# Optimization experiments

Hardware: AMD Instinct MI355X
Metric: run time of the kernel (lower is better)

The kernel has to match this reference:

```python
import jax, jax.numpy as jnp
import numpy as np

N = 1_000_000          # number of RoIs
C = 4                  # num_class (foreground classes)
IMG_H, IMG_W = 1080.0, 1920.0
BBOX_MEAN = jnp.array([0.0, 0.0, 0.0, 0.0], jnp.float32)
BBOX_STD = jnp.array([0.1, 0.1, 0.2, 0.2], jnp.float32)
THR_OBJ = 0.2          # threshold_objectness
THR_CLS = 0.1          # thresholds[0]
MIN_W, MIN_H = 6.0, 6.0
MAX_CAND = 300         # nms max_candidate_n
OVERLAP = 0.5          # nms overlap_ratio
TOP_N = 100            # nms top_n


def setup_inputs() -> dict:
    key = jax.random.key(0)
    k1, k2, k3, k4, k5 = jax.random.split(key, 5)
    logits = jax.random.normal(k1, (N, C + 1), jnp.float32) * 2.0
    cls_score_softmax = jax.nn.softmax(logits, axis=-1)          # rows sum to 1, like softmax output
    bbox_pred = jax.random.normal(k2, (N, 4 * (C + 1)), jnp.float32) * 0.5
    x1 = jax.random.uniform(k3, (N,), jnp.float32, 0.0, IMG_W * 0.8)
    y1 = jax.random.uniform(k4, (N,), jnp.float32, 0.0, IMG_H * 0.8)
    wh = jax.random.uniform(k5, (N, 2), jnp.float32, 8.0, 200.0)
    rois = jnp.stack([jnp.zeros((N,), jnp.float32), x1, y1, x1 + wh[:, 0], y1 + wh[:, 1]], axis=1)
    im_info = jnp.array([IMG_H, IMG_W], jnp.float32)
    return {"cls_score_softmax": cls_score_softmax, "bbox_pred": bbox_pred, "rois": rois, "im_info": im_info}


def _pairwise_iou(b):
    # torchvision box_iou convention: area = (x2-x1)*(y2-y1), no +1
    lt = jnp.maximum(b[:, None, :2], b[None, :, :2])
    rb = jnp.minimum(b[:, None, 2:], b[None, :, 2:])
    wh = jnp.clip(rb - lt, 0.0)
    inter = wh[..., 0] * wh[..., 1]
    area = (b[:, 2] - b[:, 0]) * (b[:, 3] - b[:, 1])
    return inter / (area[:, None] + area[None, :] - inter)


def _forward(cls_score_softmax, bbox_pred, rois, im_info):
    h_img, w_img = im_info[0], im_info[1]
    # denormalize deltas and decode against rois (bbox_transform_inv_rcnn)
    deltas = (bbox_pred.reshape(-1, 4) * BBOX_STD + BBOX_MEAN).reshape(-1, C + 1, 4)
    bx = rois[:, 1:]
    w = bx[:, 2] - bx[:, 0] + 1.0
    h = bx[:, 3] - bx[:, 1] + 1.0
    cx = bx[:, 0] + 0.5 * (w - 1.0)
    cy = bx[:, 1] + 0.5 * (h - 1.0)
    pcx = deltas[:, :, 0] * w[:, None] + cx[:, None]
    pcy = deltas[:, :, 1] * h[:, None] + cy[:, None]
    pw = jnp.exp(deltas[:, :, 2]) * w[:, None]
    ph = jnp.exp(deltas[:, :, 3]) * h[:, None]
    pred = jnp.stack([pcx - 0.5 * (pw - 1.0), pcy - 0.5 * (ph - 1.0),
                      pcx + 0.5 * (pw - 1.0), pcy + 0.5 * (ph - 1.0)], axis=-1)  # [N, C+1, 4]
    # refine_out_of_map_bbox: clip to image
    pred = jnp.stack([jnp.clip(pred[..., 0], 0.0, w_img - 1.0),
                      jnp.clip(pred[..., 1], 0.0, h_img - 1.0),
                      jnp.clip(pred[..., 2], 0.0, w_img - 1.0),
                      jnp.clip(pred[..., 3], 0.0, h_img - 1.0)], axis=-1)
    # objectness + class-score filters (masked instead of compacted: jit-friendly)
    mask_obj = (1.0 - cls_score_softmax[:, 0]) >= THR_OBJ
    maxes = jnp.max(cls_score_softmax[:, 1:], axis=1)
    argmaxes = jnp.argmax(cls_score_softmax[:, 1:], axis=1) + 1
    mask_cls = maxes > THR_CLS
    # select the box of the argmax class per row
    box = jnp.take_along_axis(pred, argmaxes[:, None, None], axis=1)[:, 0, :]  # [N, 4]
    bw = box[:, 2] - box[:, 0] + 1.0
    bh = box[:, 3] - box[:, 1] + 1.0
    mask_size = (bw >= MIN_W) | (bh >= MIN_H)  # HEIGHT_OR_WIDTH
    valid = mask_obj & mask_cls & mask_size
    # top-k candidates by max class prob (invalid rows pushed below any real score)
    cand_scores = jnp.where(valid, maxes, -1.0)
    top_vals, top_idx = jax.lax.top_k(cand_scores, MAX_CAND)   # sorted descending
    cand_boxes = box[top_idx]                                   # [M, 4]
    cand_probs = cls_score_softmax[top_idx]                     # [M, C+1]
    cand_valid = top_vals > -0.5
    # greedy NMS over the (score-sorted) candidates
    iou = _pairwise_iou(cand_boxes)
    idx = jnp.arange(MAX_CAND)

    def body(i, keep):
        sup = keep[i] & (iou[i] > OVERLAP) & (idx > i)
        return keep & ~sup

    keep = jax.lax.fori_loop(0, MAX_CAND, body, cand_valid)
    # compact kept rows into the first TOP_N slots (drop-row scatter trick)
    order = jnp.cumsum(keep.astype(jnp.int32)) - 1
    slot = jnp.where(keep & (order < TOP_N), order, TOP_N)
    rows = jnp.concatenate([jnp.zeros((MAX_CAND, 1), cand_boxes.dtype), cand_boxes, cand_probs], axis=1)
    out = jnp.zeros((TOP_N + 1, rows.shape[1]), rows.dtype).at[slot].set(rows)[:TOP_N]
    return out  # [TOP_N, 1 + 4 + (C+1)] = [100, 10], zero-padded past the kept count


def reference(cls_score_softmax, bbox_pred, rois, im_info):
    return _forward(cls_score_softmax, bbox_pred, rois, im_info)
```

## Files before the change

### kernel.cpp

```cpp
#include <hip/hip_runtime.h>
#include <math.h>

#define NBINS 4096
#define CAP   4096
#define MAXC  300
#define MAXCP 320
#define TOPN  100

__device__ __forceinline__ void decode4(float x1, float y1, float x2, float y2,
                                        float4 d4, float Wimg, float Himg,
                                        float& bx1, float& by1, float& bx2, float& by2)
{
    float w  = x2 - x1 + 1.0f;
    float h  = y2 - y1 + 1.0f;
    float cx = x1 + 0.5f*(w - 1.0f);
    float cy = y1 + 0.5f*(h - 1.0f);
    float d0 = d4.x*0.1f, d1 = d4.y*0.1f, d2 = d4.z*0.2f, d3 = d4.w*0.2f;
    float pcx = d0*w + cx;
    float pcy = d1*h + cy;
    float pw  = expf(d2)*w;
    float ph  = expf(d3)*h;
    bx1 = fminf(fmaxf(pcx - 0.5f*(pw-1.0f), 0.0f), Wimg-1.0f);
    by1 = fminf(fmaxf(pcy - 0.5f*(ph-1.0f), 0.0f), Himg-1.0f);
    bx2 = fminf(fmaxf(pcx + 0.5f*(pw-1.0f), 0.0f), Wimg-1.0f);
    by2 = fminf(fmaxf(pcy + 0.5f*(ph-1.0f), 0.0f), Himg-1.0f);
}

__global__ __launch_bounds__(256)
void rcnn_pass1(const float4* __restrict__ cls4, const float4* __restrict__ bbox4,
                const float4* __restrict__ rois4, const float* __restrict__ iminfo,
                float4* __restrict__ scores4,
                unsigned int* __restrict__ hist, unsigned int* __restrict__ counter, int Ng)
{
    if (blockIdx.x == 0) {
        for (int k = threadIdx.x; k < NBINS; k += 256) hist[k] = 0u;
        if (threadIdx.x == 0) *counter = 0u;
    }

    int g = blockIdx.x * blockDim.x + threadIdx.x;
    if (g >= Ng) return;

    float c[20], q[20];
    #pragma unroll
    for (int v = 0; v < 5; v++) {
        float4 cv = cls4[5*g + v];
        c[4*v] = cv.x; c[4*v+1] = cv.y; c[4*v+2] = cv.z; c[4*v+3] = cv.w;
        float4 rv = rois4[5*g + v];
        q[4*v] = rv.x; q[4*v+1] = rv.y; q[4*v+2] = rv.z; q[4*v+3] = rv.w;
    }
    float Himg = iminfo[0], Wimg = iminfo[1];

    float s[4];
    #pragma unroll
    for (int j = 0; j < 4; j++) {
        float p0 = c[5*j], p1 = c[5*j+1], p2 = c[5*j+2], p3 = c[5*j+3], p4 = c[5*j+4];
        float m = p1; int a = 1;
        if (p2 > m) { m = p2; a = 2; }
        if (p3 > m) { m = p3; a = 3; }
        if (p4 > m) { m = p4; a = 4; }
        float sc = -1.0f;
        if (((1.0f - p0) >= 0.2f) && (m > 0.1f)) {
            float4 d4 = bbox4[20*g + 5*j + a];
            float bx1, by1, bx2, by2;
            decode4(q[5*j+1], q[5*j+2], q[5*j+3], q[5*j+4], d4, Wimg, Himg, bx1, by1, bx2, by2);
            float bw = bx2 - bx1 + 1.0f;
            float bh = by2 - by1 + 1.0f;
            if ((bw >= 6.0f) || (bh >= 6.0f)) sc = m;
        }
        s[j] = sc;
    }
    scores4[g] = make_float4(s[0], s[1], s[2], s[3]);
}

__global__ __launch_bounds__(1024)
void rcnn_hist(const float4* __restrict__ scores4, unsigned int* __restrict__ hist, int Ng)
{
    __shared__ unsigned int lh[NBINS];
    const int t = threadIdx.x;
    for (int k = t; k < NBINS; k += 1024) lh[k] = 0u;
    __syncthreads();

    int stride = gridDim.x * 1024;
    for (int g = blockIdx.x * 1024 + t; g < Ng; g += stride) {
        float4 s4 = scores4[g];
        float ss[4] = { s4.x, s4.y, s4.z, s4.w };
        #pragma unroll
        for (int j = 0; j < 4; j++) {
            float s = ss[j];
            if (s > -0.5f) {
                int bin = (int)(s * (float)NBINS);
                bin = bin > NBINS-1 ? NBINS-1 : bin;
                atomicAdd(&lh[bin], 1u);
            }
        }
    }
    __syncthreads();
    for (int k = t; k < NBINS; k += 1024) {
        unsigned int v = lh[k];
        if (v) atomicAdd(&hist[k], v);
    }
}

__global__ __launch_bounds__(1024)
void rcnn_pass2(const unsigned int* __restrict__ hist, int* __restrict__ taubin)
{
    __shared__ unsigned int suf[1024];
    __shared__ int g_sh;
    int t = threadIdx.x;
    unsigned int v = hist[4*t] + hist[4*t+1] + hist[4*t+2] + hist[4*t+3];
    suf[t] = v;
    __syncthreads();
    for (int d = 1; d < 1024; d <<= 1) {
        unsigned int add = (t + d < 1024) ? suf[t + d] : 0u;
        __syncthreads();
        suf[t] += add;
        __syncthreads();
    }
    if (t == 0) g_sh = -1;
    __syncthreads();
    if (suf[t] >= MAXC && (t == 1023 || suf[t+1] < MAXC)) g_sh = t;
    __syncthreads();
    if (t == 0) {
        int g = g_sh;
        int tau = 0;
        if (g >= 0) {
            unsigned int cum = (g == 1023) ? 0u : suf[g+1];
            tau = 4*g;
            for (int k = 3; k >= 0; k--) {
                cum += hist[4*g + k];
                if (cum >= MAXC) { tau = 4*g + k; break; }
            }
        }
        *taubin = tau;
    }
}

__global__ __launch_bounds__(256)
void rcnn_pass3(const float4* __restrict__ scores4, const int* __restrict__ taubin,
                float* __restrict__ cscore, int* __restrict__ cidx,
                unsigned int* __restrict__ counter, int Ng)
{
    int g = blockIdx.x * blockDim.x + threadIdx.x;
    if (g >= Ng) return;
    float4 s4 = scores4[g];
    int tau = *taubin;
    float ss[4] = { s4.x, s4.y, s4.z, s4.w };
    #pragma unroll
    for (int j = 0; j < 4; j++) {
        float s = ss[j];
        if (s > -0.5f) {
            int bin = (int)(s * (float)NBINS);
            bin = bin > NBINS-1 ? NBINS-1 : bin;
            if (bin >= tau) {
                unsigned int pos = atomicAdd(counter, 1u);
                if (pos < CAP) { cscore[pos] = s; cidx[pos] = 4*g + j; }
            }
        }
    }
}

__global__ __launch_bounds__(1024)
void rcnn_final(const float* __restrict__ cls, const float* __restrict__ bbox,
                const float* __restrict__ rois, const float* __restrict__ iminfo,
                const float* __restrict__ cscore, const int* __restrict__ cidx,
                const unsigned int* __restrict__ counter, float* __restrict__ out)
{
    __shared__ __align__(16) float s_s[CAP];
    __shared__ __align__(16) int   s_id[CAP];
    __shared__ int   tid_[MAXC];
    __shared__ float bx_[MAXCP][4];
    __shared__ float areaA_[MAXCP];
    __shared__ float pr_[MAXC][5];
    __shared__ unsigned long long sup[MAXC][5];
    __shared__ unsigned long long maskw[5];
    __shared__ float orows[TOPN*10];
    __shared__ int   kept_list[TOPN];
    __shared__ int   s_kept;
    const int t  = threadIdx.x;
    const int NT = 1024;
    int M = (int)*counter; if (M > CAP) M = CAP;

    for (int i = t; i < M; i += NT)  { s_s[i] = cscore[i]; s_id[i] = cidx[i]; }
    for (int r = t; r < MAXC; r += NT) tid_[r] = -1;
    for (int r = t; r < MAXCP; r += NT) {
        bx_[r][0]=0.0f; bx_[r][1]=0.0f; bx_[r][2]=0.0f; bx_[r][3]=0.0f; areaA_[r]=0.0f;
    }
    if (t < 5) maskw[t] = 0ull;
    for (int k = t; k < TOPN*10; k += NT) orows[k] = 0.0f;
    __syncthreads();

    {
        const float4* sv = (const float4*)s_s;
        const int4*   dv = (const int4*)s_id;
        int M4 = M >> 2;
        for (int i = t; i < M; i += NT) {
            float si = s_s[i]; int di = s_id[i];
            int r = 0;
            for (int jj = 0; jj < M4; jj++) {
                float4 sj = sv[jj]; int4 dj = dv[jj];
                r += (sj.x > si) || (sj.x == si && dj.x < di);
                r += (sj.y > si) || (sj.y == si && dj.y < di);
                r += (sj.z > si) || (sj.z == si && dj.z < di);
                r += (sj.w > si) || (sj.w == si && dj.w < di);
            }
            for (int j = M4 << 2; j < M; j++) {
                float sj = s_s[j]; int dj = s_id[j];
                r += (sj > si) || (sj == si && dj < di);
            }
            if (r < MAXC) tid_[r] = di;
        }
    }
    __syncthreads();

    float Himg = iminfo[0], Wimg = iminfo[1];
    for (int r = t; r < MAXC; r += NT) {
        int i = tid_[r];
        if (i >= 0) {
            float p0 = cls[5*i], p1 = cls[5*i+1], p2 = cls[5*i+2], p3 = cls[5*i+3], p4 = cls[5*i+4];
            pr_[r][0]=p0; pr_[r][1]=p1; pr_[r][2]=p2; pr_[r][3]=p3; pr_[r][4]=p4;
            float m = p1; int a = 1;
            if (p2 > m) { m = p2; a = 2; }
            if (p3 > m) { m = p3; a = 3; }
            if (p4 > m) { m = p4; a = 4; }
            float4 d4 = ((const float4*)bbox)[5*i + a];
            float bx1, by1, bx2, by2;
            decode4(rois[5*i+1], rois[5*i+2], rois[5*i+3], rois[5*i+4], d4, Wimg, Himg, bx1, by1, bx2, by2);
            bx_[r][0]=bx1; bx_[r][1]=by1; bx_[r][2]=bx2; bx_[r][3]=by2;
            areaA_[r] = (bx2-bx1)*(by2-by1);
            atomicOr(&maskw[r>>6], 1ull << (r & 63));
        }
    }
    __syncthreads();

    for (int task = t; task < MAXC*5; task += NT) {
        int w = task / MAXC;
        int i = task - w*MAXC;
        unsigned long long bits = 0ull;
        int j0 = w << 6;
        if (j0 + 63 > i) {
            float ax1 = bx_[i][0], ay1 = bx_[i][1], ax2 = bx_[i][2], ay2 = bx_[i][3];
            float areaA = areaA_[i];
            for (int b = 0; b < 64; b++) {
                int j = j0 + b;
                float lx = fmaxf(ax1, bx_[j][0]), ly = fmaxf(ay1, bx_[j][1]);
                float rx = fminf(ax2, bx_[j][2]), ry = fminf(ay2, bx_[j][3]);
                float iw = fmaxf(rx - lx, 0.0f), ih = fmaxf(ry - ly, 0.0f);
                float inter = iw * ih;
                float iou = inter / (areaA + areaA_[j] - inter);
                bits |= (iou > 0.5f) ? (1ull << b) : 0ull;
            }
            unsigned long long jgt = (i < j0) ? ~0ull
                                  : ((i - j0) >= 63 ? 0ull : ~((1ull << (i - j0 + 1)) - 1ull));
            bits &= jgt & maskw[w];
        }
        sup[i][w] = bits;
    }
    __syncthreads();

    if (t == 0) {
        unsigned long long k0=maskw[0], k1=maskw[1], k2=maskw[2], k3=maskw[3], k4=maskw[4];
        int kept = 0;
        #define SCAN_WORD(W, KW)                                                   \
        if (kept < TOPN) {                                                         \
            unsigned long long donem = 0ull;                                       \
            for (;;) {                                                             \
                unsigned long long rem = (KW) & ~donem;                            \
                if (!rem) break;                                                   \
                int b = __builtin_ctzll(rem);                                      \
                int i = (W << 6) + b;                                              \
                kept_list[kept++] = i;                                             \
                if (kept >= TOPN) break;                                           \
                unsigned long long s0 = sup[i][0], s1 = sup[i][1], s2 = sup[i][2], \
                                   s3 = sup[i][3], s4 = sup[i][4];                 \
                k0 &= ~s0; k1 &= ~s1; k2 &= ~s2; k3 &= ~s3; k4 &= ~s4;             \
                donem = (b == 63) ? ~0ull : ((2ull << b) - 1ull);                  \
            }                                                                      \
        }
        SCAN_WORD(0, k0)
        SCAN_WORD(1, k1)
        SCAN_WORD(2, k2)
        SCAN_WORD(3, k3)
        SCAN_WORD(4, k4)
        #undef SCAN_WORD
        s_kept = kept;
    }
    __syncthreads();

    int kept = s_kept;
    if (t < kept) {
        int r = kept_list[t];
        float* row = &orows[t*10];
        row[0] = 0.0f;
        row[1] = bx_[r][0]; row[2] = bx_[r][1]; row[3] = bx_[r][2]; row[4] = bx_[r][3];
        row[5] = pr_[r][0]; row[6] = pr_[r][1]; row[7] = pr_[r][2]; row[8] = pr_[r][3]; row[9] = pr_[r][4];
    }
    __syncthreads();
    for (int k = t; k < TOPN*10; k += NT) out[k] = orows[k];
}

extern "C" void kernel_launch(void* const* d_in, const int* in_sizes, int n_in,
                              void* d_out, int out_size, void* d_ws, size_t ws_size,
                              hipStream_t stream)
{
    const float* cls    = (const float*)d_in[0];
    const float* bbox   = (const float*)d_in[1];
    const float* rois   = (const float*)d_in[2];
    const float* iminfo = (const float*)d_in[3];
    int N  = in_sizes[0] / 5;
    int Ng = N / 4;

    char* ws = (char*)d_ws;
    float* scores = (float*)ws;
    size_t off = ((size_t)N * 4 + 255) & ~(size_t)255;
    unsigned int* hist    = (unsigned int*)(ws + off); off += NBINS * 4;
    int*          taubin  = (int*)(ws + off);          off += 256;
    unsigned int* counter = (unsigned int*)(ws + off); off += 256;
    float*        cscore  = (float*)(ws + off);        off += CAP * 4;
    int*          cidx    = (int*)(ws + off);          off += CAP * 4;

    int blocksG = (Ng + 255) / 256;
    rcnn_pass1<<<blocksG, 256, 0, stream>>>((const float4*)cls, (const float4*)bbox,
                                            (const float4*)rois, iminfo,
                                            (float4*)scores, hist, counter, Ng);
    rcnn_hist<<<64, 1024, 0, stream>>>((const float4*)scores, hist, Ng);
    rcnn_pass2<<<1, 1024, 0, stream>>>(hist, taubin);
    rcnn_pass3<<<blocksG, 256, 0, stream>>>((const float4*)scores, taubin,
                                            cscore, cidx, counter, Ng);
    rcnn_final<<<1, 1024, 0, stream>>>(cls, bbox, rois, iminfo,
                                       cscore, cidx, counter, (float*)d_out);
}
```

Baseline: 213.2 us.

## Split final NMS kernel into rank, multi-block IoU mask, and scan kernels

The single-block final kernel is split into three launches: rank/decode writes boxes, areas and probabilities to workspace, a multi-block kernel computes the IoU suppression bitmasks across many CUs, and a single-block kernel runs the greedy scan and writes the output. The threshold-finding pass is also rewritten as a single-wavefront kernel that uses shuffles and a ballot instead of a shared-memory scan with many barriers. This spreads the IoU work across the GPU and cuts synchronisation in pass2, at the cost of two extra kernel launches and global-memory round trips.

```diff
diff --git a/kernel.cpp b/kernel.cpp
--- a/kernel.cpp
+++ b/kernel.cpp
@@ -5,6 +5,7 @@
 #define CAP   4096
 #define MAXC  300
 #define MAXCP 320
+#define NTASK (MAXC*5)
 #define TOPN  100
 
 __device__ __forceinline__ void decode4(float x1, float y1, float x2, float y2,
@@ -101,38 +102,41 @@
     }
 }
 
-__global__ __launch_bounds__(1024)
+__global__ __launch_bounds__(64)
 void rcnn_pass2(const unsigned int* __restrict__ hist, int* __restrict__ taubin)
 {
-    __shared__ unsigned int suf[1024];
-    __shared__ int g_sh;
-    int t = threadIdx.x;
-    unsigned int v = hist[4*t] + hist[4*t+1] + hist[4*t+2] + hist[4*t+3];
-    suf[t] = v;
-    __syncthreads();
-    for (int d = 1; d < 1024; d <<= 1) {
-        unsigned int add = (t + d < 1024) ? suf[t + d] : 0u;
-        __syncthreads();
-        suf[t] += add;
-        __syncthreads();
-    }
-    if (t == 0) g_sh = -1;
-    __syncthreads();
-    if (suf[t] >= MAXC && (t == 1023 || suf[t+1] < MAXC)) g_sh = t;
-    __syncthreads();
-    if (t == 0) {
-        int g = g_sh;
-        int tau = 0;
-        if (g >= 0) {
-            unsigned int cum = (g == 1023) ? 0u : suf[g+1];
-            tau = 4*g;
-            for (int k = 3; k >= 0; k--) {
-                cum += hist[4*g + k];
-                if (cum >= MAXC) { tau = 4*g + k; break; }
-            }
-        }
+    const int t = threadIdx.x;
+    const uint4* h4 = (const uint4*)hist;
+    uint4 v[16];
+    #pragma unroll
+    for (int j = 0; j < 16; j++) v[j] = h4[t*16 + j];
+    unsigned int chunk = 0;
+    #pragma unroll
+    for (int j = 0; j < 16; j++) chunk += v[j].x + v[j].y + v[j].z + v[j].w;
+
+    unsigned int sfx = chunk;
+    #pragma unroll
+    for (int d = 1; d < 64; d <<= 1) {
+        unsigned int o = __shfl_down(sfx, d, 64);
+        if (t + d < 64) sfx += o;
+    }
+    unsigned int nxt = sfx - chunk;
+    bool found = (sfx >= MAXC) && (nxt < MAXC);
+    unsigned long long bal = __ballot(found);
+    if (found) {
+        unsigned int cum = nxt;
+        int tau = 64*t;
+        #pragma unroll
+        for (int k = 15; k >= 0; k--) {
+            cum += v[k].w; if (cum >= MAXC) { tau = 64*t + 4*k + 3; goto done; }
+            cum += v[k].z; if (cum >= MAXC) { tau = 64*t + 4*k + 2; goto done; }
+            cum += v[k].y; if (cum >= MAXC) { tau = 64*t + 4*k + 1; goto done; }
+            cum += v[k].x; if (cum >= MAXC) { tau = 64*t + 4*k + 0; goto done; }
+        }
+        done:
         *taubin = tau;
     }
+    if (bal == 0ull && t == 0) *taubin = 0;
 }
 
 __global__ __launch_bounds__(256)
@@ -160,33 +164,24 @@
 }
 
 __global__ __launch_bounds__(1024)
-void rcnn_final(const float* __restrict__ cls, const float* __restrict__ bbox,
-                const float* __restrict__ rois, const float* __restrict__ iminfo,
-                const float* __restrict__ cscore, const int* __restrict__ cidx,
-                const unsigned int* __restrict__ counter, float* __restrict__ out)
+void rcnn_rank(const float* __restrict__ cls, const float* __restrict__ bbox,
+               const float* __restrict__ rois, const float* __restrict__ iminfo,
+               const float* __restrict__ cscore, const int* __restrict__ cidx,
+               const unsigned int* __restrict__ counter,
+               float4* __restrict__ bxg, float* __restrict__ areag,
+               float* __restrict__ prg, unsigned long long* __restrict__ maskg)
 {
     __shared__ __align__(16) float s_s[CAP];
     __shared__ __align__(16) int   s_id[CAP];
-    __shared__ int   tid_[MAXC];
-    __shared__ float bx_[MAXCP][4];
-    __shared__ float areaA_[MAXCP];
-    __shared__ float pr_[MAXC][5];
-    __shared__ unsigned long long sup[MAXC][5];
+    __shared__ int tid_[MAXC];
     __shared__ unsigned long long maskw[5];
-    __shared__ float orows[TOPN*10];
-    __shared__ int   kept_list[TOPN];
-    __shared__ int   s_kept;
     const int t  = threadIdx.x;
     const int NT = 1024;
     int M = (int)*counter; if (M > CAP) M = CAP;
 
     for (int i = t; i < M; i += NT)  { s_s[i] = cscore[i]; s_id[i] = cidx[i]; }
     for (int r = t; r < MAXC; r += NT) tid_[r] = -1;
-    for (int r = t; r < MAXCP; r += NT) {
-        bx_[r][0]=0.0f; bx_[r][1]=0.0f; bx_[r][2]=0.0f; bx_[r][3]=0.0f; areaA_[r]=0.0f;
-    }
     if (t < 5) maskw[t] = 0ull;
-    for (int k = t; k < TOPN*10; k += NT) orows[k] = 0.0f;
     __syncthreads();
 
     {
@@ -213,11 +208,13 @@
     __syncthreads();
 
     float Himg = iminfo[0], Wimg = iminfo[1];
-    for (int r = t; r < MAXC; r += NT) {
-        int i = tid_[r];
+    for (int r = t; r < MAXCP; r += NT) {
+        int i = (r < MAXC) ? tid_[r] : -1;
+        float4 bx = make_float4(0.0f, 0.0f, 0.0f, 0.0f);
+        float ar = 0.0f;
         if (i >= 0) {
             float p0 = cls[5*i], p1 = cls[5*i+1], p2 = cls[5*i+2], p3 = cls[5*i+3], p4 = cls[5*i+4];
-            pr_[r][0]=p0; pr_[r][1]=p1; pr_[r][2]=p2; pr_[r][3]=p3; pr_[r][4]=p4;
+            prg[5*r+0]=p0; prg[5*r+1]=p1; prg[5*r+2]=p2; prg[5*r+3]=p3; prg[5*r+4]=p4;
             float m = p1; int a = 1;
             if (p2 > m) { m = p2; a = 2; }
             if (p3 > m) { m = p3; a = 3; }
@@ -225,36 +222,73 @@
             float4 d4 = ((const float4*)bbox)[5*i + a];
             float bx1, by1, bx2, by2;
             decode4(rois[5*i+1], rois[5*i+2], rois[5*i+3], rois[5*i+4], d4, Wimg, Himg, bx1, by1, bx2, by2);
-            bx_[r][0]=bx1; bx_[r][1]=by1; bx_[r][2]=bx2; bx_[r][3]=by2;
-            areaA_[r] = (bx2-bx1)*(by2-by1);
+            bx = make_float4(bx1, by1, bx2, by2);
+            ar = (bx2-bx1)*(by2-by1);
             atomicOr(&maskw[r>>6], 1ull << (r & 63));
         }
-    }
-    __syncthreads();
-
-    for (int task = t; task < MAXC*5; task += NT) {
-        int w = task / MAXC;
-        int i = task - w*MAXC;
-        unsigned long long bits = 0ull;
-        int j0 = w << 6;
-        if (j0 + 63 > i) {
-            float ax1 = bx_[i][0], ay1 = bx_[i][1], ax2 = bx_[i][2], ay2 = bx_[i][3];
-            float areaA = areaA_[i];
-            for (int b = 0; b < 64; b++) {
-                int j = j0 + b;
-                float lx = fmaxf(ax1, bx_[j][0]), ly = fmaxf(ay1, bx_[j][1]);
-                float rx = fminf(ax2, bx_[j][2]), ry = fminf(ay2, bx_[j][3]);
-                float iw = fmaxf(rx - lx, 0.0f), ih = fmaxf(ry - ly, 0.0f);
-                float inter = iw * ih;
-                float iou = inter / (areaA + areaA_[j] - inter);
-                bits |= (iou > 0.5f) ? (1ull << b) : 0ull;
-            }
-            unsigned long long jgt = (i < j0) ? ~0ull
-                                  : ((i - j0) >= 63 ? 0ull : ~((1ull << (i - j0 + 1)) - 1ull));
-            bits &= jgt & maskw[w];
-        }
-        sup[i][w] = bits;
-    }
+        bxg[r] = bx; areag[r] = ar;
+    }
+    __syncthreads();
+    if (t < 5) maskg[t] = maskw[t];
+}
+
+__global__ __launch_bounds__(64)
+void rcnn_sup(const float4* __restrict__ bxg, const float* __restrict__ areag,
+              const unsigned long long* __restrict__ maskg,
+              unsigned long long* __restrict__ supg)
+{
+    __shared__ float4 bxs[MAXCP];
+    __shared__ float  ars[MAXCP];
+    const int t = threadIdx.x;
+    for (int r = t; r < MAXCP; r += 64) { bxs[r] = bxg[r]; ars[r] = areag[r]; }
+    __syncthreads();
+
+    int task = blockIdx.x * 64 + t;
+    if (task >= NTASK) return;
+    int w = task / MAXC;
+    int i = task - w * MAXC;
+    unsigned long long bits = 0ull;
+    int j0 = w << 6;
+    if (j0 + 63 > i) {
+        float4 bi = bxs[i];
+        float areaA = ars[i];
+        for (int b = 0; b < 64; b++) {
+            int j = j0 + b;
+            float4 bj = bxs[j];
+            float lx = fmaxf(bi.x, bj.x), ly = fmaxf(bi.y, bj.y);
+            float rx = fminf(bi.z, bj.z), ry = fminf(bi.w, bj.w);
+            float iw = fmaxf(rx - lx, 0.0f), ih = fmaxf(ry - ly, 0.0f);
+            float inter = iw * ih;
+            float iou = inter / (areaA + ars[j] - inter);
+            bits |= (iou > 0.5f) ? (1ull << b) : 0ull;
+        }
+        unsigned long long jgt = (i < j0) ? ~0ull
+                              : ((i - j0) >= 63 ? 0ull : ~((1ull << (i - j0 + 1)) - 1ull));
+        bits &= jgt & maskg[w];
+    }
+    supg[i*6 + w] = bits;
+}
+
+__global__ __launch_bounds__(1024)
+void rcnn_scan(const float4* __restrict__ bxg, const float* __restrict__ prg,
+               const unsigned long long* __restrict__ maskg,
+               const unsigned long long* __restrict__ supg, float* __restrict__ out)
+{
+    __shared__ __align__(16) unsigned long long sup[MAXC*6];
+    __shared__ unsigned long long maskw[5];
+    __shared__ float orows[TOPN*10];
+    __shared__ int   kept_list[TOPN];
+    __shared__ int   s_kept;
+    const int t  = threadIdx.x;
+    const int NT = 1024;
+
+    {
+        const ulonglong2* sg2 = (const ulonglong2*)supg;
+        ulonglong2* sl2 = (ulonglong2*)sup;
+        for (int k = t; k < (MAXC*6)/2; k += NT) sl2[k] = sg2[k];
+    }
+    if (t < 5) maskw[t] = maskg[t];
+    for (int k = t; k < TOPN*10; k += NT) orows[k] = 0.0f;
     __syncthreads();
 
     if (t == 0) {
@@ -270,8 +304,9 @@
                 int i = (W << 6) + b;                                              \
                 kept_list[kept++] = i;                                             \
                 if (kept >= TOPN) break;                                           \
-                unsigned long long s0 = sup[i][0], s1 = sup[i][1], s2 = sup[i][2], \
-                                   s3 = sup[i][3], s4 = sup[i][4];                 \
+                unsigned long long s0 = sup[i*6+0], s1 = sup[i*6+1],               \
+                                   s2 = sup[i*6+2], s3 = sup[i*6+3],               \
+                                   s4 = sup[i*6+4];                                \
                 k0 &= ~s0; k1 &= ~s1; k2 &= ~s2; k3 &= ~s3; k4 &= ~s4;             \
                 donem = (b == 63) ? ~0ull : ((2ull << b) - 1ull);                  \
             }                                                                      \
@@ -289,10 +324,12 @@
     int kept = s_kept;
     if (t < kept) {
         int r = kept_list[t];
+        float4 bx = bxg[r];
         float* row = &orows[t*10];
         row[0] = 0.0f;
-        row[1] = bx_[r][0]; row[2] = bx_[r][1]; row[3] = bx_[r][2]; row[4] = bx_[r][3];
-        row[5] = pr_[r][0]; row[6] = pr_[r][1]; row[7] = pr_[r][2]; row[8] = pr_[r][3]; row[9] = pr_[r][4];
+        row[1] = bx.x; row[2] = bx.y; row[3] = bx.z; row[4] = bx.w;
+        row[5] = prg[5*r+0]; row[6] = prg[5*r+1]; row[7] = prg[5*r+2];
+        row[8] = prg[5*r+3]; row[9] = prg[5*r+4];
     }
     __syncthreads();
     for (int k = t; k < TOPN*10; k += NT) out[k] = orows[k];
@@ -317,15 +354,23 @@
     unsigned int* counter = (unsigned int*)(ws + off); off += 256;
     float*        cscore  = (float*)(ws + off);        off += CAP * 4;
     int*          cidx    = (int*)(ws + off);          off += CAP * 4;
+    float4*       bxg     = (float4*)(ws + off);       off += MAXCP * 16;
+    float*        areag   = (float*)(ws + off);        off += ((MAXCP * 4 + 255) & ~(size_t)255);
+    float*        prg     = (float*)(ws + off);        off += ((MAXC * 5 * 4 + 255) & ~(size_t)255);
+    unsigned long long* maskg = (unsigned long long*)(ws + off); off += 256;
+    unsigned long long* supg  = (unsigned long long*)(ws + off); off += MAXC * 6 * 8;
 
     int blocksG = (Ng + 255) / 256;
     rcnn_pass1<<<blocksG, 256, 0, stream>>>((const float4*)cls, (const float4*)bbox,
                                             (const float4*)rois, iminfo,
                                             (float4*)scores, hist, counter, Ng);
     rcnn_hist<<<64, 1024, 0, stream>>>((const float4*)scores, hist, Ng);
-    rcnn_pass2<<<1, 1024, 0, stream>>>(hist, taubin);
+    rcnn_pass2<<<1, 64, 0, stream>>>(hist, taubin);
     rcnn_pass3<<<blocksG, 256, 0, stream>>>((const float4*)scores, taubin,
                                             cscore, cidx, counter, Ng);
-    rcnn_final<<<1, 1024, 0, stream>>>(cls, bbox, rois, iminfo,
-                                       cscore, cidx, counter, (float*)d_out);
-}
+    rcnn_rank<<<1, 1024, 0, stream>>>(cls, bbox, rois, iminfo,
+                                      cscore, cidx, counter,
+                                      bxg, areag, prg, maskg);
+    rcnn_sup<<<(NTASK + 63) / 64, 64, 0, stream>>>(bxg, areag, maskg, supg);
+    rcnn_scan<<<1, 1024, 0, stream>>>(bxg, prg, maskg, supg, (float*)d_out);
+}
```

Measured after the change: 206.5 us. 3.2% less time.
